# Kernel tuning notes

Measured on AMD Instinct MI355X. Metric: run time of the kernel, lower is better.

Reference implementation:

```python
import jax, jax.numpy as jnp
import numpy as np

B, S, H, D = 4, 2048, 16, 1024  # batch, seq, heads, n_units
DK = D // H


def setup_inputs() -> dict:
    key = jax.random.key(0)
    ks = jax.random.split(key, 12)
    k_init = float(np.sqrt(1.0 / D))
    u = lambda k, shape: jax.random.uniform(k, shape, jnp.float32, -k_init, k_init)
    # causal mask, shared across batch/heads (True = attend)
    mask = jnp.broadcast_to(jnp.tril(jnp.ones((S, S), dtype=bool)), (B, S, S))
    return {
        "query": jax.random.normal(ks[0], (B, S, D), jnp.float32),
        "key": jax.random.normal(ks[1], (B, S, D), jnp.float32),
        "value": jax.random.normal(ks[2], (B, S, D), jnp.float32),
        "Wq": u(ks[3], (H, DK, D)), "bq": u(ks[4], (H, DK)),
        "Wk": u(ks[5], (H, DK, D)), "bk": u(ks[6], (H, DK)),
        "Wv": u(ks[7], (H, DK, D)), "bv": u(ks[8], (H, DK)),
        "Wp": u(ks[9], (D, D)), "bp": u(ks[10], (D,)),
        "mask": mask,
    }


def reference(query, key, value, Wq, bq, Wk, bk, Wv, bv, Wp, bp, mask):
    # per-head projections, batched over heads: [B,S,D] x [H,DK,D] -> [B,H,S,DK]
    Q = jnp.einsum('bsd,hkd->bhsk', query, Wq) + bq[None, :, None, :]
    K = jnp.einsum('bsd,hkd->bhsk', key, Wk) + bk[None, :, None, :]
    V = jnp.einsum('bsd,hkd->bhsk', value, Wv) + bv[None, :, None, :]
    scores = jnp.einsum('bhsk,bhtk->bhst', Q, K) / jnp.sqrt(jnp.float32(DK))
    scores = jnp.where(mask[:, None, :, :], scores, jnp.float32(-1e9))
    attn = jax.nn.softmax(scores, axis=-1)  # dropout disabled (eval)
    Z = jnp.einsum('bhst,bhtk->bhsk', attn, V)
    # concat heads on feature dim: [B,S,H*DK]
    Z = jnp.transpose(Z, (0, 2, 1, 3)).reshape(B, S, D)
    return Z @ Wp.T + bp
```

## Files before the change

### kernel.cpp

```cpp
#include <hip/hip_runtime.h>

typedef __bf16 bf16;
typedef __bf16 bf16x8 __attribute__((ext_vector_type(8)));
typedef float f32x4 __attribute__((ext_vector_type(4)));

#define BB 4
#define SS 2048
#define HH 16
#define DD 1024
#define DK 64
#define MTOT (BB * SS)

#define C1 0.18033688f
#define C2 -11.5415603f

__device__ __forceinline__ void gl_lds16(const bf16* g, bf16* l)
{
    __builtin_amdgcn_global_load_lds(
        (const __attribute__((address_space(1))) unsigned int*)g,
        (__attribute__((address_space(3))) unsigned int*)l, 16, 0, 0);
}

__global__ __launch_bounds__(256) void conv_kernel(
    const float* __restrict__ q, const float* __restrict__ k,
    const float* __restrict__ v,
    const float* __restrict__ wq, const float* __restrict__ wk,
    const float* __restrict__ wv, const float* __restrict__ wp,
    bf16* __restrict__ xdst, bf16* __restrict__ wdst)
{
    const float* src; bf16* d; size_t i;
    if (blockIdx.z < 3) {
        src = (blockIdx.z == 0) ? q : (blockIdx.z == 1) ? k : v;
        d = xdst + (size_t)blockIdx.z * ((size_t)MTOT * DD);
        i = ((size_t)blockIdx.x * 256 + threadIdx.x) * 8;
    } else {
        if (blockIdx.x >= 2048) return;
        const int wsel = blockIdx.x >> 9;
        src = (wsel == 0) ? wq : (wsel == 1) ? wk : (wsel == 2) ? wv : wp;
        d = wdst + (size_t)wsel * ((size_t)DD * DD);
        i = ((size_t)(blockIdx.x & 511) * 256 + threadIdx.x) * 8;
    }
    const float4 v0 = *(const float4*)(src + i);
    const float4 v1 = *(const float4*)(src + i + 4);
    bf16x8 r = { (bf16)v0.x, (bf16)v0.y, (bf16)v0.z, (bf16)v0.w,
                 (bf16)v1.x, (bf16)v1.y, (bf16)v1.z, (bf16)v1.w };
    *(bf16x8*)(d + i) = r;
}

__global__ __launch_bounds__(256) void gemm_qkv(
    const bf16* __restrict__ x0, const bf16* __restrict__ x1,
    const bf16* __restrict__ x2, const bf16* __restrict__ w0,
    const bf16* __restrict__ w1, const bf16* __restrict__ w2,
    const float* __restrict__ bias0, const float* __restrict__ bias1,
    const float* __restrict__ bias2,
    bf16* __restrict__ o0, bf16* __restrict__ o1, bf16* __restrict__ o2)
{
    __shared__ __align__(16) bf16 smem[128 * 32 * 2];
    bf16* As = smem;
    bf16* Bs = smem + 128 * 32;

    const int z = blockIdx.z;
    const bf16* A = (z == 0) ? x0 : (z == 1) ? x1 : x2;
    const bf16* W = (z == 0) ? w0 : (z == 1) ? w1 : w2;
    const float* bias = (z == 0) ? bias0 : (z == 1) ? bias1 : bias2;
    bf16* out = (z == 0) ? o0 : (z == 1) ? o1 : o2;

    const int tid  = threadIdx.x;
    const int wave = tid >> 6;
    const int lane = tid & 63;
    const int quad = lane >> 4;
    const int lr   = lane & 15;
    const int wm   = wave >> 1;
    const int wn   = wave & 1;

    const int m_base = blockIdx.y * 128;
    const int n_base = blockIdx.x * 128;
    const int srow = lane >> 2;
    const int scol = (lane & 3) * 8;

    f32x4 acc[4][4];
    #pragma unroll
    for (int i = 0; i < 4; ++i)
        #pragma unroll
        for (int j = 0; j < 4; ++j)
            acc[i][j] = (f32x4){0.f, 0.f, 0.f, 0.f};

    for (int k0 = 0; k0 < DD; k0 += 32) {
        #pragma unroll
        for (int seg = wave; seg < 16; seg += 4) {
            if (seg < 8)
                gl_lds16(A + (size_t)(m_base + seg * 16 + srow) * DD + k0 + scol,
                         As + seg * 512);
            else
                gl_lds16(W + (size_t)(n_base + (seg - 8) * 16 + srow) * DD + k0 + scol,
                         Bs + (seg - 8) * 512);
        }
        __syncthreads();

        bf16x8 af[4], bfr[4];
        #pragma unroll
        for (int i = 0; i < 4; ++i)
            af[i] = *(const bf16x8*)&As[(wm * 64 + i * 16 + lr) * 32 + quad * 8];
        #pragma unroll
        for (int j = 0; j < 4; ++j)
            bfr[j] = *(const bf16x8*)&Bs[(wn * 64 + j * 16 + lr) * 32 + quad * 8];

        #pragma unroll
        for (int i = 0; i < 4; ++i)
            #pragma unroll
            for (int j = 0; j < 4; ++j)
                acc[i][j] = __builtin_amdgcn_mfma_f32_16x16x32_bf16(
                                af[i], bfr[j], acc[i][j], 0, 0, 0);
        __syncthreads();
    }

    if (z == 2) {
        bf16* e = smem + wave * 1216;
        const int h  = (n_base + wn * 64) >> 6;
        const int mg = m_base + wm * 64;
        const int b  = mg >> 11;
        const int s0 = mg & (SS - 1);
        #pragma unroll
        for (int j = 0; j < 4; ++j) {
            const float bb = bias[n_base + wn * 64 + j * 16 + lr];
            #pragma unroll
            for (int i = 0; i < 4; ++i)
                #pragma unroll
                for (int r = 0; r < 4; ++r)
                    e[lr * 76 + i * 16 + quad * 4 + r] = (bf16)(acc[i][j][r] + bb);
            #pragma unroll
            for (int p = 0; p < 2; ++p) {
                const int nn = p * 8 + (lane >> 3);
                const int mm = (lane & 7) * 8;
                const bf16x8 vv = *(const bf16x8*)&e[nn * 76 + mm];
                const int dk = j * 16 + nn;
                *(bf16x8*)(out + ((size_t)(b * HH + h) * DK + dk) * SS + s0 + mm) = vv;
            }
        }
    } else {
        #pragma unroll
        for (int j = 0; j < 4; ++j) {
            const int n  = n_base + wn * 64 + j * 16 + lr;
            const float bb = bias[n];
            const int h  = n >> 6;
            const int dk = n & (DK - 1);
            #pragma unroll
            for (int i = 0; i < 4; ++i)
                #pragma unroll
                for (int r = 0; r < 4; ++r) {
                    const int m = m_base + wm * 64 + i * 16 + quad * 4 + r;
                    const int bi = m >> 11, s = m & (SS - 1);
                    out[(((size_t)bi * HH + h) * SS + s) * DK + dk]
                        = (bf16)(acc[i][j][r] + bb);
                }
        }
    }
}

__global__ __launch_bounds__(256) void gemm_out(
    const bf16* __restrict__ A, const bf16* __restrict__ W,
    const float* __restrict__ bias, float* __restrict__ out)
{
    __shared__ __align__(16) bf16 As[128 * 32];
    __shared__ __align__(16) bf16 Bs[64 * 32];

    const int tid  = threadIdx.x;
    const int wave = tid >> 6;
    const int lane = tid & 63;
    const int quad = lane >> 4;
    const int lr   = lane & 15;

    const int m_base = blockIdx.y * 128;
    const int n_base = blockIdx.x * 64;
    const int srow = lane >> 2;
    const int scol = (lane & 3) * 8;

    f32x4 acc[2][4];
    #pragma unroll
    for (int i = 0; i < 2; ++i)
        #pragma unroll
        for (int j = 0; j < 4; ++j)
            acc[i][j] = (f32x4){0.f, 0.f, 0.f, 0.f};

    for (int k0 = 0; k0 < DD; k0 += 32) {
        #pragma unroll
        for (int seg = wave; seg < 12; seg += 4) {
            if (seg < 8)
                gl_lds16(A + (size_t)(m_base + seg * 16 + srow) * DD + k0 + scol,
                         As + seg * 512);
            else
                gl_lds16(W + (size_t)(n_base + (seg - 8) * 16 + srow) * DD + k0 + scol,
                         Bs + (seg - 8) * 512);
        }
        __syncthreads();

        bf16x8 af[2], bfr[4];
        #pragma unroll
        for (int i = 0; i < 2; ++i)
            af[i] = *(const bf16x8*)&As[(wave * 32 + i * 16 + lr) * 32 + quad * 8];
        #pragma unroll
        for (int j = 0; j < 4; ++j)
            bfr[j] = *(const bf16x8*)&Bs[(j * 16 + lr) * 32 + quad * 8];

        #pragma unroll
        for (int i = 0; i < 2; ++i)
            #pragma unroll
            for (int j = 0; j < 4; ++j)
                acc[i][j] = __builtin_amdgcn_mfma_f32_16x16x32_bf16(
                                af[i], bfr[j], acc[i][j], 0, 0, 0);
        __syncthreads();
    }

    #pragma unroll
    for (int j = 0; j < 4; ++j) {
        const int n = n_base + j * 16 + lr;
        const float bb = bias[n];
        #pragma unroll
        for (int i = 0; i < 2; ++i)
            #pragma unroll
            for (int r = 0; r < 4; ++r) {
                const int m = m_base + wave * 32 + i * 16 + quad * 4 + r;
                out[(size_t)m * DD + n] = acc[i][j][r] + bb;
            }
    }
}

template <bool DIAG>
__device__ __forceinline__ void attn_tile4(
    int quad, int lr, const bf16* __restrict__ Kc, const bf16* __restrict__ Vc,
    bf16* __restrict__ pb, const bf16x8 aq[2][2], const bf16x8& ones,
    f32x4 acc[2][4], f32x4 acc_l[2])
{
    bf16x8 kb[2][2];
    #pragma unroll
    for (int kvh = 0; kvh < 2; ++kvh)
        #pragma unroll
        for (int kc = 0; kc < 2; ++kc)
            kb[kvh][kc] = *(const bf16x8*)&Kc[
                ((kvh * 16 + lr) * 8 + ((kc * 4 + quad) ^ (lr & 7))) * 8];
    bf16x8 vb[4];
    #pragma unroll
    for (int c = 0; c < 4; ++c)
        vb[c] = *(const bf16x8*)&Vc[
            ((c * 16 + lr) * 4 + (quad ^ ((lr >> 1) & 3))) * 8];

    f32x4 s[2][2];
    #pragma unroll
    for (int h = 0; h < 2; ++h)
        #pragma unroll
        for (int kvh = 0; kvh < 2; ++kvh) {
            s[h][kvh] = (f32x4){0.f, 0.f, 0.f, 0.f};
            s[h][kvh] = __builtin_amdgcn_mfma_f32_16x16x32_bf16(
                            aq[h][0], kb[kvh][0], s[h][kvh], 0, 0, 0);
            s[h][kvh] = __builtin_amdgcn_mfma_f32_16x16x32_bf16(
                            aq[h][1], kb[kvh][1], s[h][kvh], 0, 0, 0);
        }

    #pragma unroll
    for (int h = 0; h < 2; ++h)
        #pragma unroll
        for (int kvh = 0; kvh < 2; ++kvh)
            #pragma unroll
            for (int r = 0; r < 4; ++r) {
                float p = exp2f(fmaf(s[h][kvh][r], C1, C2));
                if constexpr (DIAG) {
                    const bool ok = (kvh * 16 + lr) <= (h * 16 + quad * 4 + r);
                    p = ok ? p : 0.0f;
                }
                pb[(h * 16 + quad * 4 + r) * 40 + kvh * 16 + lr] = (bf16)p;
            }

    bf16x8 ap[2];
    #pragma unroll
    for (int h = 0; h < 2; ++h)
        ap[h] = *(const bf16x8*)&pb[(h * 16 + lr) * 40 + quad * 8];

    #pragma unroll
    for (int h = 0; h < 2; ++h)
        acc_l[h] = __builtin_amdgcn_mfma_f32_16x16x32_bf16(
                        ap[h], ones, acc_l[h], 0, 0, 0);
    #pragma unroll
    for (int c = 0; c < 4; ++c)
        #pragma unroll
        for (int h = 0; h < 2; ++h)
            acc[h][c] = __builtin_amdgcn_mfma_f32_16x16x32_bf16(
                            ap[h], vb[c], acc[h][c], 0, 0, 0);
}

__global__ __launch_bounds__(256, 4) void attn_kernel4(
    const bf16* __restrict__ q_ws, const bf16* __restrict__ k_ws,
    const bf16* __restrict__ v_ws, bf16* __restrict__ z_ws)
{
    __shared__ __align__(16) bf16 Kst[2][32 * 64];
    __shared__ __align__(16) bf16 Vst[2][64 * 32];
    __shared__ __align__(16) bf16 pbuf[4][32 * 40];

    const int tid  = threadIdx.x;
    const int w    = tid >> 6;
    const int lane = tid & 63;
    const int quad = lane >> 4;
    const int lr   = lane & 15;

    const int bh = blockIdx.x & 63;
    const int qg = 15 - (blockIdx.x >> 6);
    const int m0 = qg * 128 + w * 32;
    const int lim = 4 * qg + w;
    const int ntiles = 4 * qg + 4;

    const size_t base = (size_t)bh * SS * DK;
    const bf16* Kb = k_ws + base;
    const bf16* Vb = v_ws + base;
    bf16* pb = pbuf[w];

    const int krow = w * 8 + (lane >> 3);
    const int kcc  = (lane & 7) ^ ((lane >> 3) & 7);
    const bf16* ksrc = Kb + (size_t)krow * DK + kcc * 8;
    const int vrow = w * 16 + (lane >> 2);
    const int vcc  = (lane & 3) ^ ((lane >> 3) & 3);
    const bf16* vsrc = Vb + (size_t)vrow * SS + vcc * 8;

    bf16x8 aq[2][2];
    #pragma unroll
    for (int h = 0; h < 2; ++h)
        #pragma unroll
        for (int kc = 0; kc < 2; ++kc)
            aq[h][kc] = *(const bf16x8*)(q_ws + base
                + (size_t)(m0 + h * 16 + lr) * DK + kc * 32 + quad * 8);

    bf16x8 ones;
    #pragma unroll
    for (int i = 0; i < 8; ++i) ones[i] = (bf16)1.0f;

    f32x4 acc[2][4], acc_l[2];
    #pragma unroll
    for (int h = 0; h < 2; ++h) {
        acc_l[h] = (f32x4){0.f, 0.f, 0.f, 0.f};
        #pragma unroll
        for (int c = 0; c < 4; ++c) acc[h][c] = (f32x4){0.f, 0.f, 0.f, 0.f};
    }

    gl_lds16(ksrc, &Kst[0][w * 512]);
    gl_lds16(vsrc, &Vst[0][w * 512]);
    __syncthreads();

    for (int t = 0; t < ntiles; ++t) {
        if (t + 1 < ntiles) {
            gl_lds16(ksrc + (size_t)(t + 1) * 32 * DK, &Kst[(t + 1) & 1][w * 512]);
            gl_lds16(vsrc + (t + 1) * 32,              &Vst[(t + 1) & 1][w * 512]);
        }
        const bf16* Kc = Kst[t & 1];
        const bf16* Vc = Vst[t & 1];
        if (t < lim)
            attn_tile4<false>(quad, lr, Kc, Vc, pb, aq, ones, acc, acc_l);
        else if (t == lim)
            attn_tile4<true>(quad, lr, Kc, Vc, pb, aq, ones, acc, acc_l);
        __syncthreads();
    }

    const int b = bh >> 4, hh = bh & (HH - 1);
    #pragma unroll
    for (int h = 0; h < 2; ++h)
        #pragma unroll
        for (int r = 0; r < 4; ++r) {
            const float inv = 1.0f / acc_l[h][r];
            const int s = m0 + h * 16 + quad * 4 + r;
            #pragma unroll
            for (int c = 0; c < 4; ++c)
                z_ws[((size_t)(b * SS + s)) * DD + hh * DK + c * 16 + lr]
                    = (bf16)(acc[h][c][r] * inv);
        }
}

extern "C" void kernel_launch(void* const* d_in, const int* in_sizes, int n_in,
                              void* d_out, int out_size, void* d_ws, size_t ws_size,
                              hipStream_t stream)
{
    const float* query = (const float*)d_in[0];
    const float* key_  = (const float*)d_in[1];
    const float* value = (const float*)d_in[2];
    const float* Wq = (const float*)d_in[3];
    const float* bq = (const float*)d_in[4];
    const float* Wk = (const float*)d_in[5];
    const float* bk = (const float*)d_in[6];
    const float* Wv = (const float*)d_in[7];
    const float* bv = (const float*)d_in[8];
    const float* Wp = (const float*)d_in[9];
    const float* bp = (const float*)d_in[10];

    const size_t X = (size_t)MTOT * DD;
    const size_t W = (size_t)DD * DD;
    bf16* xq  = (bf16*)d_ws;
    bf16* xk  = xq + X;
    bf16* xv  = xk + X;
    bf16* wqb = xv + X;
    bf16* wkb = wqb + W;
    bf16* wvb = wkb + W;
    bf16* wpb = wvb + W;
    bf16* q_ws = wpb + W;
    bf16* k_ws = q_ws + X;
    bf16* v_ws = k_ws + X;
    bf16* z_ws = xq;

    conv_kernel<<<dim3(4096, 1, 4), 256, 0, stream>>>(
        query, key_, value, Wq, Wk, Wv, Wp, xq, wqb);

    gemm_qkv<<<dim3(8, 64, 3), 256, 0, stream>>>(
        xq, xk, xv, wqb, wkb, wvb, bq, bk, bv, q_ws, k_ws, v_ws);

    attn_kernel4<<<dim3(1024), 256, 0, stream>>>(q_ws, k_ws, v_ws, z_ws);

    gemm_out<<<dim3(16, 64), 256, 0, stream>>>(z_ws, wpb, bp, (float*)d_out);
}
```

Baseline: 370.9 us.

## Rewrite QKV GEMM with 256x256 tiles, double-buffered LDS, and swizzled layout

The QKV projection GEMM moves from 128x128 tiles with 4 waves and a single-stage synchronous loop to 256x256 tiles with 8 waves. A K-step of 64 is double-buffered in 128 KB of LDS, with the next tile's global->LDS loads interleaved between MFMA phases. An XOR swizzle is added to avoid LDS bank conflicts, and s_setprio is raised around the MFMA bursts. The aim is to hide global load latency and raise arithmetic intensity, at the cost of more registers, a large LDS footprint, and fewer blocks in the grid.

Measured after the change: 368.3 us. Within noise of the previous version (-0.7%).

```diff
diff --git a/kernel.cpp b/kernel.cpp
--- a/kernel.cpp
+++ b/kernel.cpp
@@ -47,7 +47,37 @@
     *(bf16x8*)(d + i) = r;
 }
 
-__global__ __launch_bounds__(256) void gemm_qkv(
+template<int KC, int NH>
+__device__ __forceinline__ void qphase(
+    const bf16* __restrict__ sb, int wm, int wn, int lr, int swz8,
+    bf16x8 a[8], f32x4 acc[8][4],
+    const bf16* __restrict__ ssrc, bf16* __restrict__ sdst, bool doStage)
+{
+    if constexpr (NH == 0) {
+        #pragma unroll
+        for (int i = 0; i < 8; ++i)
+            a[i] = *(const bf16x8*)&sb[KC * 8192 + (wm * 128 + i * 16 + lr) * 32 + swz8];
+    }
+    bf16x8 b0 = *(const bf16x8*)&sb[16384 + KC * 8192 + (wn * 64 + (NH * 2 + 0) * 16 + lr) * 32 + swz8];
+    bf16x8 b1 = *(const bf16x8*)&sb[16384 + KC * 8192 + (wn * 64 + (NH * 2 + 1) * 16 + lr) * 32 + swz8];
+    __builtin_amdgcn_s_barrier();
+    asm volatile("s_waitcnt lgkmcnt(0)" ::: "memory");
+    __builtin_amdgcn_s_setprio(1);
+    #pragma unroll
+    for (int i = 0; i < 8; ++i) {
+        acc[i][NH * 2 + 0] = __builtin_amdgcn_mfma_f32_16x16x32_bf16(
+                                 a[i], b0, acc[i][NH * 2 + 0], 0, 0, 0);
+        acc[i][NH * 2 + 1] = __builtin_amdgcn_mfma_f32_16x16x32_bf16(
+                                 a[i], b1, acc[i][NH * 2 + 1], 0, 0, 0);
+    }
+    __builtin_amdgcn_s_setprio(0);
+    if (doStage) {
+        gl_lds16(ssrc, sdst);
+        gl_lds16(ssrc + (size_t)128 * DD, sdst + 4096);
+    }
+}
+
+__global__ __launch_bounds__(512, 2) void gemm_qkv(
     const bf16* __restrict__ x0, const bf16* __restrict__ x1,
     const bf16* __restrict__ x2, const bf16* __restrict__ w0,
     const bf16* __restrict__ w1, const bf16* __restrict__ w2,
@@ -55,9 +85,7 @@
     const float* __restrict__ bias2,
     bf16* __restrict__ o0, bf16* __restrict__ o1, bf16* __restrict__ o2)
 {
-    __shared__ __align__(16) bf16 smem[128 * 32 * 2];
-    bf16* As = smem;
-    bf16* Bs = smem + 128 * 32;
+    __shared__ __align__(16) bf16 smem[2 * 32768];
 
     const int z = blockIdx.z;
     const bf16* A = (z == 0) ? x0 : (z == 1) ? x1 : x2;
@@ -66,75 +94,87 @@
     bf16* out = (z == 0) ? o0 : (z == 1) ? o1 : o2;
 
     const int tid  = threadIdx.x;
-    const int wave = tid >> 6;
+    const int w    = tid >> 6;
     const int lane = tid & 63;
     const int quad = lane >> 4;
     const int lr   = lane & 15;
-    const int wm   = wave >> 1;
-    const int wn   = wave & 1;
-
-    const int m_base = blockIdx.y * 128;
-    const int n_base = blockIdx.x * 128;
-    const int srow = lane >> 2;
-    const int scol = (lane & 3) * 8;
-
-    f32x4 acc[4][4];
-    #pragma unroll
-    for (int i = 0; i < 4; ++i)
+    const int wm   = w >> 2;
+    const int wn   = w & 3;
+
+    const int m_base = blockIdx.y * 256;
+    const int n_base = blockIdx.x * 256;
+    const int swz8 = (quad ^ ((lr >> 1) & 3)) * 8;
+
+    const int c0 = ((tid & 3) ^ ((tid >> 3) & 3)) * 8;
+    const bf16* srcA = A + (size_t)(m_base + (tid >> 2)) * DD + c0;
+    const bf16* srcB = W + (size_t)(n_base + (tid >> 2)) * DD + c0;
+
+    f32x4 acc[8][4];
+    #pragma unroll
+    for (int i = 0; i < 8; ++i)
         #pragma unroll
         for (int j = 0; j < 4; ++j)
             acc[i][j] = (f32x4){0.f, 0.f, 0.f, 0.f};
-
-    for (int k0 = 0; k0 < DD; k0 += 32) {
-        #pragma unroll
-        for (int seg = wave; seg < 16; seg += 4) {
-            if (seg < 8)
-                gl_lds16(A + (size_t)(m_base + seg * 16 + srow) * DD + k0 + scol,
-                         As + seg * 512);
-            else
-                gl_lds16(W + (size_t)(n_base + (seg - 8) * 16 + srow) * DD + k0 + scol,
-                         Bs + (seg - 8) * 512);
-        }
-        __syncthreads();
-
-        bf16x8 af[4], bfr[4];
-        #pragma unroll
-        for (int i = 0; i < 4; ++i)
-            af[i] = *(const bf16x8*)&As[(wm * 64 + i * 16 + lr) * 32 + quad * 8];
-        #pragma unroll
-        for (int j = 0; j < 4; ++j)
-            bfr[j] = *(const bf16x8*)&Bs[(wn * 64 + j * 16 + lr) * 32 + quad * 8];
-
-        #pragma unroll
-        for (int i = 0; i < 4; ++i)
-            #pragma unroll
-            for (int j = 0; j < 4; ++j)
-                acc[i][j] = __builtin_amdgcn_mfma_f32_16x16x32_bf16(
-                                af[i], bfr[j], acc[i][j], 0, 0, 0);
-        __syncthreads();
+    bf16x8 a[8];
+
+    #pragma unroll
+    for (int t = 0; t < 2; ++t) {
+        bf16* db = smem + t * 32768;
+        #pragma unroll
+        for (int kc = 0; kc < 2; ++kc) {
+            const bf16* sA = srcA + t * 64 + kc * 32;
+            const bf16* sB = srcB + t * 64 + kc * 32;
+            gl_lds16(sA,                      db + kc * 8192 + w * 512);
+            gl_lds16(sA + (size_t)128 * DD,   db + kc * 8192 + 4096 + w * 512);
+            gl_lds16(sB,                      db + 16384 + kc * 8192 + w * 512);
+            gl_lds16(sB + (size_t)128 * DD,   db + 16384 + kc * 8192 + 4096 + w * 512);
+        }
+    }
+    asm volatile("s_waitcnt vmcnt(8)" ::: "memory");
+    __builtin_amdgcn_s_barrier();
+
+    #pragma unroll 2
+    for (int T = 0; T < 16; ++T) {
+        const bf16* sb = smem + (T & 1) * 32768;
+        bf16* db = smem + (T & 1) * 32768;
+        const bool st = (T + 2 < 16);
+        const int tn = st ? (T + 2) : 0;
+        const bf16* sA = srcA + tn * 64;
+        const bf16* sB = srcB + tn * 64;
+
+        qphase<0, 0>(sb, wm, wn, lr, swz8, a, acc, sA,      db + w * 512,                 st);
+        __builtin_amdgcn_s_barrier();
+        qphase<0, 1>(sb, wm, wn, lr, swz8, a, acc, sB,      db + 16384 + w * 512,         st);
+        __builtin_amdgcn_s_barrier();
+        qphase<1, 0>(sb, wm, wn, lr, swz8, a, acc, sA + 32, db + 8192 + w * 512,          st);
+        __builtin_amdgcn_s_barrier();
+        qphase<1, 1>(sb, wm, wn, lr, swz8, a, acc, sB + 32, db + 16384 + 8192 + w * 512,  st);
+        if (st) asm volatile("s_waitcnt vmcnt(8)" ::: "memory");
+        else    asm volatile("s_waitcnt vmcnt(0)" ::: "memory");
+        __builtin_amdgcn_s_barrier();
     }
 
     if (z == 2) {
-        bf16* e = smem + wave * 1216;
-        const int h  = (n_base + wn * 64) >> 6;
-        const int mg = m_base + wm * 64;
+        bf16* e = smem + w * 2176;
+        const int hh = (n_base + wn * 64) >> 6;
+        const int mg = m_base + wm * 128;
         const int b  = mg >> 11;
         const int s0 = mg & (SS - 1);
         #pragma unroll
         for (int j = 0; j < 4; ++j) {
             const float bb = bias[n_base + wn * 64 + j * 16 + lr];
             #pragma unroll
-            for (int i = 0; i < 4; ++i)
+            for (int i = 0; i < 8; ++i)
                 #pragma unroll
                 for (int r = 0; r < 4; ++r)
-                    e[lr * 76 + i * 16 + quad * 4 + r] = (bf16)(acc[i][j][r] + bb);
-            #pragma unroll
-            for (int p = 0; p < 2; ++p) {
-                const int nn = p * 8 + (lane >> 3);
-                const int mm = (lane & 7) * 8;
-                const bf16x8 vv = *(const bf16x8*)&e[nn * 76 + mm];
+                    e[lr * 136 + i * 16 + quad * 4 + r] = (bf16)(acc[i][j][r] + bb);
+            #pragma unroll
+            for (int p = 0; p < 4; ++p) {
+                const int nn = p * 4 + quad;
+                const int mm = lr * 8;
+                const bf16x8 vv = *(const bf16x8*)&e[nn * 136 + mm];
                 const int dk = j * 16 + nn;
-                *(bf16x8*)(out + ((size_t)(b * HH + h) * DK + dk) * SS + s0 + mm) = vv;
+                *(bf16x8*)(out + ((size_t)(b * HH + hh) * DK + dk) * SS + s0 + mm) = vv;
             }
         }
     } else {
@@ -142,15 +182,15 @@
         for (int j = 0; j < 4; ++j) {
             const int n  = n_base + wn * 64 + j * 16 + lr;
             const float bb = bias[n];
-            const int h  = n >> 6;
+            const int hh = n >> 6;
             const int dk = n & (DK - 1);
             #pragma unroll
-            for (int i = 0; i < 4; ++i)
+            for (int i = 0; i < 8; ++i)
                 #pragma unroll
                 for (int r = 0; r < 4; ++r) {
-                    const int m = m_base + wm * 64 + i * 16 + quad * 4 + r;
+                    const int m = m_base + wm * 128 + i * 16 + quad * 4 + r;
                     const int bi = m >> 11, s = m & (SS - 1);
-                    out[(((size_t)bi * HH + h) * SS + s) * DK + dk]
+                    out[(((size_t)bi * HH + hh) * SS + s) * DK + dk]
                         = (bf16)(acc[i][j][r] + bb);
                 }
         }
@@ -404,7 +444,7 @@
     conv_kernel<<<dim3(4096, 1, 4), 256, 0, stream>>>(
         query, key_, value, Wq, Wk, Wv, Wp, xq, wqb);
 
-    gemm_qkv<<<dim3(8, 64, 3), 256, 0, stream>>>(
+    gemm_qkv<<<dim3(4, 32, 3), 512, 0, stream>>>(
         xq, xk, xv, wqb, wkb, wvb, bq, bk, bv, q_ws, k_ws, v_ws);
 
     attn_kernel4<<<dim3(1024), 256, 0, stream>>>(q_ws, k_ws, v_ws, z_ws);
```
